# Kernel optimization log

Hardware: AMD Instinct MI355X
Metric: run time of the kernel (lower is better)

The kernel has to match this reference:

```python
import jax, jax.numpy as jnp
import numpy as np

D_MODEL = 1024
M = 4
NUM_EXPERTS = 8
TOP_K = 2
B, T = 2, 2048


def setup_inputs() -> dict:
    key = jax.random.key(0)
    ks = jax.random.split(key, 4)
    d_ff = D_MODEL * M
    x = jax.random.normal(ks[0], (B, T, D_MODEL), dtype=jnp.float32)
    # torch nn.Linear(d_model, num_experts, bias=False): stored here as (D, E) so logits = x @ gate_w
    gate_w = jax.random.normal(ks[1], (D_MODEL, NUM_EXPERTS), dtype=jnp.float32) * 0.02
    w1 = jax.random.normal(ks[2], (NUM_EXPERTS, D_MODEL, d_ff), dtype=jnp.float32) * 0.02
    b1 = jnp.zeros((NUM_EXPERTS, d_ff), dtype=jnp.float32)
    w2 = jax.random.normal(ks[3], (NUM_EXPERTS, d_ff, D_MODEL), dtype=jnp.float32) * 0.02
    b2 = jnp.zeros((NUM_EXPERTS, D_MODEL), dtype=jnp.float32)
    return {"x": x, "gate_w": gate_w, "w1": w1, "b1": b1, "w2": w2, "b2": b2}


def reference(x, gate_w, w1, b1, w2, b2):
    Bb, Tt, D = x.shape
    E = w1.shape[0]
    N = Bb * Tt
    # gating: top-k logits -> softmax over the k selected experts
    logits = jnp.einsum('btd,de->bte', x, gate_w)               # (B,T,E)
    top_v, top_i = jax.lax.top_k(logits, TOP_K)                 # (B,T,K)
    top_w = jax.nn.softmax(top_v, axis=-1)                      # (B,T,K)

    xf = x.reshape(N, D)
    idx = top_i.reshape(N, TOP_K)
    wts = top_w.reshape(N, TOP_K)
    # dense combine weights: comb[n, e] = sum_k wts[n,k] * [idx[n,k]==e]
    comb = jnp.zeros((N, E), dtype=x.dtype).at[jnp.arange(N)[:, None], idx].add(wts)

    # per-expert dense 2-layer MLP (exact erf GELU, matching torch F.gelu default),
    # combined with gate weights (zero weight == token not routed to expert).
    out = jnp.zeros((N, D), dtype=x.dtype)
    for e in range(E):
        h = jax.nn.gelu(xf @ w1[e] + b1[e], approximate=False)  # (N, D*M)
        out = out + comb[:, e:e + 1] * (h @ w2[e] + b2[e])      # (N, D)
    return out.reshape(Bb, Tt, D)
```

## Files before the change

### kernel.cpp

```cpp
#include <hip/hip_runtime.h>
#include <hip/hip_bf16.h>
#include <math.h>

#define D_MODEL 1024
#define D_FF    4096
#define NEXP    8
#define NTOK    4096
#define NROUTED 8192
#define MAXJOBS 40

typedef __attribute__((ext_vector_type(8))) short bf16x8;
typedef __attribute__((ext_vector_type(4))) float f32x4;
typedef __attribute__((ext_vector_type(4))) unsigned short us4;

#define WS_CNT   0
#define WS_CNT2  64
#define WS_OFF   128
#define WS_JOBS  192
#define WS_TI    512
#define WS_TW    (WS_TI + NTOK*2*4)
#define WS_TOK   (WS_TW + NTOK*2*4)
#define WS_GWT   (WS_TOK + NROUTED*4)
#define WS_XG    (((WS_GWT + NROUTED*4) + 255) & ~255)
#define WS_H     (WS_XG + (size_t)NROUTED*D_MODEL*2)
#define WS_WT    (WS_H + (size_t)NROUTED*D_FF*2)
#define WS_WT2   (WS_WT + (size_t)NEXP*D_FF*D_MODEL*2)
#define WS_END   (WS_WT2 + (size_t)NEXP*D_FF*D_MODEL*2)

__device__ __forceinline__ unsigned short f2bf(float f){
  union { float f; unsigned u; } a; a.f = f;
  unsigned u = a.u;
  u = u + 0x7FFF + ((u >> 16) & 1);
  return (unsigned short)(u >> 16);
}

__device__ __forceinline__ void gload_lds16(const void* g, void* l){
  __builtin_amdgcn_global_load_lds((const __attribute__((address_space(1))) void*)g,
                                   (__attribute__((address_space(3))) void*)l, 16, 0, 0);
}

__global__ void moe_gate_kernel(const float* __restrict__ x, const float* __restrict__ gw,
                                int* cnt, int* __restrict__ ti, float* __restrict__ tw){
  int n = blockIdx.x*4 + (threadIdx.x >> 6);
  int lane = threadIdx.x & 63;
  const float* xr = x + (size_t)n * D_MODEL;
  float acc[NEXP];
  #pragma unroll
  for (int e=0;e<NEXP;e++) acc[e] = 0.f;
  for (int d=lane; d<D_MODEL; d+=64){
    float xv = xr[d];
    #pragma unroll
    for (int e=0;e<NEXP;e++) acc[e] += xv * gw[d*NEXP + e];
  }
  #pragma unroll
  for (int e=0;e<NEXP;e++){
    #pragma unroll
    for (int o=32;o;o>>=1) acc[e] += __shfl_down(acc[e], o, 64);
  }
  if (lane == 0){
    int i0 = 0; float v0 = acc[0];
    #pragma unroll
    for (int e=1;e<NEXP;e++) if (acc[e] > v0){ v0 = acc[e]; i0 = e; }
    int i1 = -1; float v1 = -1e30f;
    #pragma unroll
    for (int e=0;e<NEXP;e++) if (e != i0 && acc[e] > v1){ v1 = acc[e]; i1 = e; }
    float p = expf(v1 - v0);
    float inv = 1.f / (1.f + p);
    ti[n*2] = i0; ti[n*2+1] = i1;
    tw[n*2] = inv; tw[n*2+1] = p * inv;
    atomicAdd(&cnt[i0], 1); atomicAdd(&cnt[i1], 1);
  }
}

__global__ void moe_prefix_kernel(const int* __restrict__ cnt, int* __restrict__ off,
                                  int* __restrict__ jobs){
  if (threadIdx.x == 0){
    int s = 0;
    for (int e=0;e<NEXP;e++){ off[e] = s; s += cnt[e]; }
    off[NEXP] = s;
    int idx = 0;
    for (int e=0;e<NEXP;e++){
      int ns = (cnt[e] + 255) >> 8;
      for (int q=0;q<ns;q++) jobs[1+idx++] = (e<<16) | q;
    }
    jobs[0] = idx;
  }
}

__device__ __forceinline__ void assign_body(
    int n, const float* __restrict__ x, const int* __restrict__ ti,
    const float* __restrict__ tw, const int* __restrict__ off,
    int* cnt2, int* __restrict__ tok, float* __restrict__ gwt,
    unsigned short* __restrict__ Xg){
  __shared__ int ss[2];
  if (threadIdx.x == 0){
    int i0 = ti[n*2], i1 = ti[n*2+1];
    int s0 = off[i0] + atomicAdd(&cnt2[i0], 1);
    int s1 = off[i1] + atomicAdd(&cnt2[i1], 1);
    tok[s0] = n; tok[s1] = n;
    gwt[s0] = tw[n*2]; gwt[s1] = tw[n*2+1];
    ss[0] = s0; ss[1] = s1;
  }
  __syncthreads();
  int s0 = ss[0], s1 = ss[1];
  int t = threadIdx.x;
  f32x4 v = *(const f32x4*)(x + (size_t)n * D_MODEL + t*4);
  us4 pk = { f2bf(v.x), f2bf(v.y), f2bf(v.z), f2bf(v.w) };
  __builtin_nontemporal_store(pk, (us4*)(Xg + (size_t)s0 * D_MODEL + t*4));
  __builtin_nontemporal_store(pk, (us4*)(Xg + (size_t)s1 * D_MODEL + t*4));
}

__device__ __forceinline__ void transpose_tile(
    int idx, int gtid, float (*tile)[65],
    const float* __restrict__ W, unsigned short* __restrict__ Wt, int K, int F){
  int fpe = F >> 6, kpe = K >> 6;
  int e = idx / (fpe*kpe), rem = idx % (fpe*kpe);
  int f0 = (rem % fpe) * 64, k0 = (rem / fpe) * 64;
  const float* Wb = W + (size_t)e * K * F;
  unsigned short* Wtb = Wt + (size_t)e * F * K;
  #pragma unroll
  for (int i=0;i<4;i++){
    int q = i*256 + gtid;
    int r = q >> 4, c4 = (q & 15) * 4;
    f32x4 v = __builtin_nontemporal_load((const f32x4*)(Wb + (size_t)(k0 + r) * F + f0 + c4));
    tile[r][c4] = v.x; tile[r][c4+1] = v.y; tile[r][c4+2] = v.z; tile[r][c4+3] = v.w;
  }
  __syncthreads();
  #pragma unroll
  for (int i=0;i<4;i++){
    int q = i*256 + gtid;
    int f = q >> 4, k4 = (q & 15) * 4;
    us4 pk = { f2bf(tile[k4][f]), f2bf(tile[k4+1][f]), f2bf(tile[k4+2][f]), f2bf(tile[k4+3][f]) };
    __builtin_nontemporal_store(pk, (us4*)(Wtb + (size_t)(f0 + f) * K + k0 + k4));
  }
}

__global__ __launch_bounds__(256) void transpose_bf16_kernel(
    const float* W, unsigned short* Wt, int K, int F){
  __shared__ float tile[64][65];
  transpose_tile(blockIdx.x, threadIdx.x, tile, W, Wt, K, F);
}

__global__ __launch_bounds__(256) void moe_fusedA_kernel(
    const float* __restrict__ x, const int* __restrict__ ti, const float* __restrict__ tw,
    const int* __restrict__ off, int* cnt2, int* __restrict__ tok, float* __restrict__ gwt,
    unsigned short* __restrict__ Xg,
    const float* __restrict__ w1, unsigned short* __restrict__ Wt1){
  int b = blockIdx.x;
  if (b < NTOK){
    assign_body(b, x, ti, tw, off, cnt2, tok, gwt, Xg);
  } else {
    __shared__ float tile[64][65];
    transpose_tile(b - NTOK, threadIdx.x, tile, w1, Wt1, D_MODEL, D_FF);
  }
}

template<int MODE>
__global__ __launch_bounds__(1024) void moe_gemm_kernel(
    char* __restrict__ wsb, const unsigned short* __restrict__ Bt,
    const float* __restrict__ bias, float* __restrict__ out,
    const float* __restrict__ w2src, unsigned short* __restrict__ Wt2)
{
  __shared__ __align__(16) char lds[3*32768];

  if (MODE == 1 && (int)blockIdx.y >= MAXJOBS){
    int slot = ((int)blockIdx.y - MAXJOBS) * (int)gridDim.x + (int)blockIdx.x;
    int g = threadIdx.x >> 8, gtid = threadIdx.x & 255;
    float (*tiles)[64][65] = (float(*)[64][65])lds;
    transpose_tile(slot*4 + g, gtid, tiles[g], w2src, Wt2, D_FF, D_MODEL);
    return;
  }

  const int* jobs = (const int*)(wsb + WS_JOBS);
  if ((int)blockIdx.y >= jobs[0]) return;
  const int jb = jobs[1 + blockIdx.y];
  const int e = jb >> 16;
  const int row0 = (jb & 0xffff) << 8;

  const int* off = (const int*)(wsb + WS_OFF);
  const int n0 = off[e];
  const int ne = off[e+1] - n0;

  constexpr int K  = (MODE==1) ? D_MODEL : D_FF;
  constexpr int NT = (MODE==1) ? 32 : 64;
  const int bx     = (MODE==1) ? blockIdx.x : (blockIdx.x & 3);
  const int kchunk = (MODE==1) ? 0 : (blockIdx.x >> 2);
  const int n_off  = bx * 256;
  const size_t kcb = (size_t)kchunk * 4096;

  const unsigned short* Ag = (const unsigned short*)(wsb + (MODE==1 ? (size_t)WS_XG : (size_t)WS_H));

  const int tid = threadIdx.x, lane = tid & 63, w = tid >> 6;
  const int wr = w >> 2, wc = w & 3;

  const int rA   = w*16 + (lane >> 2);
  const int qs   = ((lane & 3) ^ ((rA >> 1) & 3)) << 4;
  int grA = row0 + rA; if (grA >= ne) grA = ne - 1;
  const char* aSrc = (const char*)(Ag + (size_t)(n0 + grA) * K) + kcb + qs;
  const char* bSrc = (const char*)(Bt + (size_t)e * D_FF * D_MODEL + (size_t)(n_off + rA) * K) + kcb + qs;
  const int dA = w*1024, dB = 16384 + w*1024;

  const int q0 = lane >> 4;
  int aoff[4], boff[4];
  #pragma unroll
  for (int mi=0; mi<4; mi++){
    int row = wr*64 + mi*16 + (lane & 15);
    aoff[mi] = row*64 + ((q0 ^ ((row>>1)&3)) << 4);
  }
  #pragma unroll
  for (int ni=0; ni<4; ni++){
    int col = wc*64 + ni*16 + (lane & 15);
    boff[ni] = 16384 + col*64 + ((q0 ^ ((col>>1)&3)) << 4);
  }

  f32x4 acc[4][4];
  #pragma unroll
  for (int i=0;i<4;i++)
    #pragma unroll
    for (int j=0;j<4;j++) acc[i][j] = (f32x4){0.f,0.f,0.f,0.f};

  #define STAGE(tt, ss) { \
    gload_lds16(aSrc + (size_t)(tt)*64, lds + (ss)*32768 + dA); \
    gload_lds16(bSrc + (size_t)(tt)*64, lds + (ss)*32768 + dB); }

  STAGE(0, 0);
  STAGE(1, 1);

  for (int t = 0; t < NT; ++t){
    if (t < NT-1) asm volatile("s_waitcnt vmcnt(2)" ::: "memory");
    else          asm volatile("s_waitcnt vmcnt(0)" ::: "memory");
    __builtin_amdgcn_s_barrier();
    __builtin_amdgcn_sched_barrier(0);

    if (t + 2 < NT) STAGE(t + 2, (t + 2) % 3);

    const char* base = lds + (t % 3) * 32768;
    bf16x8 a[4], b[4];
    #pragma unroll
    for (int mi=0; mi<4; mi++) a[mi] = *(const bf16x8*)(base + aoff[mi]);
    #pragma unroll
    for (int ni=0; ni<4; ni++) b[ni] = *(const bf16x8*)(base + boff[ni]);

    asm volatile("s_waitcnt lgkmcnt(0)" ::: "memory");
    __builtin_amdgcn_sched_barrier(0);
    __builtin_amdgcn_s_setprio(1);
    #pragma unroll
    for (int ni=0; ni<4; ni++)
      #pragma unroll
      for (int mi=0; mi<4; mi++)
        acc[mi][ni] = __builtin_amdgcn_mfma_f32_16x16x32_bf16(a[mi], b[ni], acc[mi][ni], 0, 0, 0);
    __builtin_amdgcn_s_setprio(0);
    __builtin_amdgcn_sched_barrier(0);
  }
  #undef STAGE

  if (MODE == 1){
    const float* b1 = bias + (size_t)e * D_FF;
    unsigned short* H = (unsigned short*)(wsb + (size_t)WS_H);
    #pragma unroll
    for (int mi=0; mi<4; mi++){
      int rbase = wr*64 + mi*16 + ((lane>>4)<<2);
      #pragma unroll
      for (int rr=0;rr<4;rr++){
        int lrow = rbase + rr;
        if (row0 + lrow < ne){
          size_t hb = (size_t)(n0 + row0 + lrow) * D_FF;
          #pragma unroll
          for (int ni=0; ni<4; ni++){
            int gcol = n_off + wc*64 + ni*16 + (lane&15);
            float v = acc[mi][ni][rr] + b1[gcol];
            v = 0.5f * v * (1.f + erff(v * 0.70710678118654752f));
            __builtin_nontemporal_store(f2bf(v), H + hb + gcol);
          }
        }
      }
    }
  } else {
    const float* b2 = bias + (size_t)e * D_MODEL;
    const int* tok = (const int*)(wsb + WS_TOK);
    const float* gwt = (const float*)(wsb + WS_GWT);
    #pragma unroll
    for (int mi=0; mi<4; mi++){
      int rbase = wr*64 + mi*16 + ((lane>>4)<<2);
      #pragma unroll
      for (int rr=0;rr<4;rr++){
        int lrow = rbase + rr;
        if (row0 + lrow < ne){
          int slot = n0 + row0 + lrow;
          int tk = tok[slot];
          float g = gwt[slot];
          float* orow = out + (size_t)tk * D_MODEL;
          #pragma unroll
          for (int ni=0; ni<4; ni++){
            int gcol = n_off + wc*64 + ni*16 + (lane&15);
            float bb = (kchunk == 0) ? b2[gcol] : 0.f;
            atomicAdd(orow + gcol, (acc[mi][ni][rr] + bb) * g);
          }
        }
      }
    }
  }
}

extern "C" void kernel_launch(void* const* d_in, const int* in_sizes, int n_in,
                              void* d_out, int out_size, void* d_ws, size_t ws_size,
                              hipStream_t stream){
  const float* x   = (const float*)d_in[0];
  const float* gw  = (const float*)d_in[1];
  const float* w1  = (const float*)d_in[2];
  const float* b1  = (const float*)d_in[3];
  const float* w2  = (const float*)d_in[4];
  const float* b2  = (const float*)d_in[5];
  float* out = (float*)d_out;
  char* ws = (char*)d_ws;
  unsigned short* Wt1 = (unsigned short*)(ws + (size_t)WS_WT);
  unsigned short* Wt2 = (unsigned short*)(ws + (size_t)WS_WT2);

  hipMemsetAsync(ws, 0, 512, stream);
  hipMemsetAsync(out, 0, (size_t)NTOK * D_MODEL * sizeof(float), stream);

  moe_gate_kernel<<<NTOK/4, 256, 0, stream>>>(x, gw, (int*)(ws+WS_CNT),
                                              (int*)(ws+WS_TI), (float*)(ws+WS_TW));
  moe_prefix_kernel<<<1, 64, 0, stream>>>((const int*)(ws+WS_CNT), (int*)(ws+WS_OFF),
                                          (int*)(ws+WS_JOBS));
  moe_fusedA_kernel<<<NTOK + 8192, 256, 0, stream>>>(
      x, (const int*)(ws+WS_TI), (const float*)(ws+WS_TW), (const int*)(ws+WS_OFF),
      (int*)(ws+WS_CNT2), (int*)(ws+WS_TOK), (float*)(ws+WS_GWT),
      (unsigned short*)(ws + (size_t)WS_XG), w1, Wt1);

  if (ws_size >= (size_t)WS_END){
    moe_gemm_kernel<1><<<dim3(D_FF/256, MAXJOBS + 128), 1024, 0, stream>>>(ws, Wt1, b1, out, w2, Wt2);
    moe_gemm_kernel<2><<<dim3((D_MODEL/256)*2, MAXJOBS), 1024, 0, stream>>>(ws, Wt2, b2, out, nullptr, nullptr);
  } else {
    moe_gemm_kernel<1><<<dim3(D_FF/256, MAXJOBS), 1024, 0, stream>>>(ws, Wt1, b1, out, nullptr, nullptr);
    transpose_bf16_kernel<<<8192, 256, 0, stream>>>(w2, Wt1, D_FF, D_MODEL);
    moe_gemm_kernel<2><<<dim3((D_MODEL/256)*2, MAXJOBS), 1024, 0, stream>>>(ws, Wt1, b2, out, nullptr, nullptr);
  }
}
```

Before: 541.7 us.

## Restructure expert GEMM to 8-wave blocks with 128-wide K double-buffered ping-pong

The expert GEMM kernel moves from 16 waves with a triple-buffered 64-wide K step to 8 waves (two blocks per CU) with a double-buffered 128-wide K step. Each wave now computes a 128x64 sub-tile, and the per-step work is split into four MFMA phases with barriers, so the next A and B tiles are staged while earlier phases compute. The aim is more MFMA work per LDS byte and per barrier, plus overlap of loads with compute, in the style of a ping-pong schedule. The cost is more accumulator registers and many more barriers per step, and the transpose side-blocks are re-gridded to match the smaller blocks.

```diff
diff --git a/kernel.cpp b/kernel.cpp
--- a/kernel.cpp
+++ b/kernel.cpp
@@ -156,18 +156,18 @@
 }
 
 template<int MODE>
-__global__ __launch_bounds__(1024) void moe_gemm_kernel(
+__global__ __launch_bounds__(512, 2) void moe_gemm_kernel(
     char* __restrict__ wsb, const unsigned short* __restrict__ Bt,
     const float* __restrict__ bias, float* __restrict__ out,
     const float* __restrict__ w2src, unsigned short* __restrict__ Wt2)
 {
-  __shared__ __align__(16) char lds[3*32768];
+  __shared__ __align__(16) char lds[2*65536];
 
   if (MODE == 1 && (int)blockIdx.y >= MAXJOBS){
     int slot = ((int)blockIdx.y - MAXJOBS) * (int)gridDim.x + (int)blockIdx.x;
     int g = threadIdx.x >> 8, gtid = threadIdx.x & 255;
     float (*tiles)[64][65] = (float(*)[64][65])lds;
-    transpose_tile(slot*4 + g, gtid, tiles[g], w2src, Wt2, D_FF, D_MODEL);
+    transpose_tile(slot*2 + g, gtid, tiles[g], w2src, Wt2, D_FF, D_MODEL);
     return;
   }
 
@@ -182,7 +182,7 @@
   const int ne = off[e+1] - n0;
 
   constexpr int K  = (MODE==1) ? D_MODEL : D_FF;
-  constexpr int NT = (MODE==1) ? 32 : 64;
+  constexpr int NT = (MODE==1) ? 16 : 32;
   const int bx     = (MODE==1) ? blockIdx.x : (blockIdx.x & 3);
   const int kchunk = (MODE==1) ? 0 : (blockIdx.x >> 2);
   const int n_off  = bx * 256;
@@ -191,75 +191,146 @@
   const unsigned short* Ag = (const unsigned short*)(wsb + (MODE==1 ? (size_t)WS_XG : (size_t)WS_H));
 
   const int tid = threadIdx.x, lane = tid & 63, w = tid >> 6;
-  const int wr = w >> 2, wc = w & 3;
-
-  const int rA   = w*16 + (lane >> 2);
-  const int qs   = ((lane & 3) ^ ((rA >> 1) & 3)) << 4;
-  int grA = row0 + rA; if (grA >= ne) grA = ne - 1;
-  const char* aSrc = (const char*)(Ag + (size_t)(n0 + grA) * K) + kcb + qs;
-  const char* bSrc = (const char*)(Bt + (size_t)e * D_FF * D_MODEL + (size_t)(n_off + rA) * K) + kcb + qs;
-  const int dA = w*1024, dB = 16384 + w*1024;
-
-  const int q0 = lane >> 4;
-  int aoff[4], boff[4];
-  #pragma unroll
-  for (int mi=0; mi<4; mi++){
-    int row = wr*64 + mi*16 + (lane & 15);
-    aoff[mi] = row*64 + ((q0 ^ ((row>>1)&3)) << 4);
-  }
-  #pragma unroll
-  for (int ni=0; ni<4; ni++){
-    int col = wc*64 + ni*16 + (lane & 15);
-    boff[ni] = 16384 + col*64 + ((q0 ^ ((col>>1)&3)) << 4);
-  }
-
-  f32x4 acc[4][4];
-  #pragma unroll
-  for (int i=0;i<4;i++)
+  const int wrM = w >> 2, wcN = w & 3;
+  const int l15 = lane & 15, q16 = (lane >> 4) << 4;
+
+  const int arow   = lane >> 3;
+  const int achunk = ((lane & 7) ^ arow) << 4;
+  const char* aP[4]; const char* bP[4];
+  #pragma unroll
+  for (int i=0;i<4;i++){
+    int r = (w*4 + i)*8 + arow;
+    int gr = row0 + r; if (gr >= ne) gr = ne - 1;
+    aP[i] = (const char*)(Ag + (size_t)(n0 + gr) * K) + kcb + achunk;
+    bP[i] = (const char*)(Bt + (size_t)e * D_FF * D_MODEL + (size_t)(n_off + r) * K) + kcb + achunk;
+  }
+  const int dstA = w*4096;
+
+  #define STAGE_A(tt, bb) { \
+    size_t kb = (size_t)(tt)*128; \
+    char* d = lds + (bb)*65536 + dstA; \
+    _Pragma("unroll") \
+    for (int i=0;i<4;i++) gload_lds16(aP[i] + kb, d + i*1024); }
+  #define STAGE_B(tt, bb) { \
+    size_t kb = (size_t)(tt)*128; \
+    char* d = lds + (bb)*65536 + 32768 + dstA; \
+    _Pragma("unroll") \
+    for (int i=0;i<4;i++) gload_lds16(bP[i] + kb, d + i*1024); }
+
+  f32x4 acc[8][4];
+  #pragma unroll
+  for (int i=0;i<8;i++)
     #pragma unroll
     for (int j=0;j<4;j++) acc[i][j] = (f32x4){0.f,0.f,0.f,0.f};
 
-  #define STAGE(tt, ss) { \
-    gload_lds16(aSrc + (size_t)(tt)*64, lds + (ss)*32768 + dA); \
-    gload_lds16(bSrc + (size_t)(tt)*64, lds + (ss)*32768 + dB); }
-
-  STAGE(0, 0);
-  STAGE(1, 1);
+  STAGE_A(0, 0); STAGE_B(0, 0);
+  asm volatile("s_waitcnt vmcnt(0)" ::: "memory");
+  __builtin_amdgcn_s_barrier();
 
   for (int t = 0; t < NT; ++t){
-    if (t < NT-1) asm volatile("s_waitcnt vmcnt(2)" ::: "memory");
-    else          asm volatile("s_waitcnt vmcnt(0)" ::: "memory");
-    __builtin_amdgcn_s_barrier();
-    __builtin_amdgcn_sched_barrier(0);
-
-    if (t + 2 < NT) STAGE(t + 2, (t + 2) % 3);
-
-    const char* base = lds + (t % 3) * 32768;
-    bf16x8 a[4], b[4];
-    #pragma unroll
-    for (int mi=0; mi<4; mi++) a[mi] = *(const bf16x8*)(base + aoff[mi]);
-    #pragma unroll
-    for (int ni=0; ni<4; ni++) b[ni] = *(const bf16x8*)(base + boff[ni]);
-
+    const char* base = lds + (t & 1) * 65536;
+    const int nb = (t & 1) ^ 1;
+    bf16x8 aF[2][4], bL[2][2], bH[2][2];
+
+    #pragma unroll
+    for (int kk=0; kk<2; ++kk){
+      #pragma unroll
+      for (int mi=0; mi<4; mi++){
+        int row = wrM*128 + mi*16 + l15;
+        aF[kk][mi] = *(const bf16x8*)(base + (row<<7) + (((kk<<6)+q16) ^ ((row&7)<<4)));
+      }
+      #pragma unroll
+      for (int ni=0; ni<2; ni++){
+        int col = wcN*64 + ni*16 + l15;
+        bL[kk][ni] = *(const bf16x8*)(base + 32768 + (col<<7) + (((kk<<6)+q16) ^ ((col&7)<<4)));
+      }
+    }
+    if (t + 1 < NT) STAGE_A(t+1, nb);
+    __builtin_amdgcn_sched_barrier(0);
+    __builtin_amdgcn_s_barrier();
     asm volatile("s_waitcnt lgkmcnt(0)" ::: "memory");
     __builtin_amdgcn_sched_barrier(0);
     __builtin_amdgcn_s_setprio(1);
     #pragma unroll
-    for (int ni=0; ni<4; ni++)
-      #pragma unroll
-      for (int mi=0; mi<4; mi++)
-        acc[mi][ni] = __builtin_amdgcn_mfma_f32_16x16x32_bf16(a[mi], b[ni], acc[mi][ni], 0, 0, 0);
+    for (int kk=0; kk<2; ++kk)
+      #pragma unroll
+      for (int ni=0; ni<2; ni++)
+        #pragma unroll
+        for (int mi=0; mi<4; mi++)
+          acc[mi][ni] = __builtin_amdgcn_mfma_f32_16x16x32_bf16(aF[kk][mi], bL[kk][ni], acc[mi][ni], 0, 0, 0);
     __builtin_amdgcn_s_setprio(0);
     __builtin_amdgcn_sched_barrier(0);
-  }
-  #undef STAGE
+    __builtin_amdgcn_s_barrier();
+
+    #pragma unroll
+    for (int kk=0; kk<2; ++kk)
+      #pragma unroll
+      for (int ni=0; ni<2; ni++){
+        int col = wcN*64 + (ni+2)*16 + l15;
+        bH[kk][ni] = *(const bf16x8*)(base + 32768 + (col<<7) + (((kk<<6)+q16) ^ ((col&7)<<4)));
+      }
+    if (t + 1 < NT) STAGE_B(t+1, nb);
+    __builtin_amdgcn_sched_barrier(0);
+    __builtin_amdgcn_s_barrier();
+    asm volatile("s_waitcnt lgkmcnt(0)" ::: "memory");
+    __builtin_amdgcn_sched_barrier(0);
+    __builtin_amdgcn_s_setprio(1);
+    #pragma unroll
+    for (int kk=0; kk<2; ++kk)
+      #pragma unroll
+      for (int ni=0; ni<2; ni++)
+        #pragma unroll
+        for (int mi=0; mi<4; mi++)
+          acc[mi][ni+2] = __builtin_amdgcn_mfma_f32_16x16x32_bf16(aF[kk][mi], bH[kk][ni], acc[mi][ni+2], 0, 0, 0);
+    __builtin_amdgcn_s_setprio(0);
+    __builtin_amdgcn_sched_barrier(0);
+    __builtin_amdgcn_s_barrier();
+
+    #pragma unroll
+    for (int kk=0; kk<2; ++kk)
+      #pragma unroll
+      for (int mi=0; mi<4; mi++){
+        int row = wrM*128 + (mi+4)*16 + l15;
+        aF[kk][mi] = *(const bf16x8*)(base + (row<<7) + (((kk<<6)+q16) ^ ((row&7)<<4)));
+      }
+    __builtin_amdgcn_sched_barrier(0);
+    __builtin_amdgcn_s_barrier();
+    asm volatile("s_waitcnt lgkmcnt(0)" ::: "memory");
+    __builtin_amdgcn_sched_barrier(0);
+    __builtin_amdgcn_s_setprio(1);
+    #pragma unroll
+    for (int kk=0; kk<2; ++kk)
+      #pragma unroll
+      for (int ni=0; ni<2; ni++)
+        #pragma unroll
+        for (int mi=0; mi<4; mi++)
+          acc[mi+4][ni] = __builtin_amdgcn_mfma_f32_16x16x32_bf16(aF[kk][mi], bL[kk][ni], acc[mi+4][ni], 0, 0, 0);
+    __builtin_amdgcn_s_setprio(0);
+    __builtin_amdgcn_sched_barrier(0);
+    __builtin_amdgcn_s_barrier();
+
+    __builtin_amdgcn_s_setprio(1);
+    #pragma unroll
+    for (int kk=0; kk<2; ++kk)
+      #pragma unroll
+      for (int ni=0; ni<2; ni++)
+        #pragma unroll
+        for (int mi=0; mi<4; mi++)
+          acc[mi+4][ni+2] = __builtin_amdgcn_mfma_f32_16x16x32_bf16(aF[kk][mi], bH[kk][ni], acc[mi+4][ni+2], 0, 0, 0);
+    __builtin_amdgcn_s_setprio(0);
+    __builtin_amdgcn_sched_barrier(0);
+    if (t + 1 < NT) asm volatile("s_waitcnt vmcnt(0)" ::: "memory");
+    __builtin_amdgcn_s_barrier();
+  }
+  #undef STAGE_A
+  #undef STAGE_B
 
   if (MODE == 1){
     const float* b1 = bias + (size_t)e * D_FF;
     unsigned short* H = (unsigned short*)(wsb + (size_t)WS_H);
     #pragma unroll
-    for (int mi=0; mi<4; mi++){
-      int rbase = wr*64 + mi*16 + ((lane>>4)<<2);
+    for (int mi=0; mi<8; mi++){
+      int rbase = wrM*128 + mi*16 + ((lane>>4)<<2);
       #pragma unroll
       for (int rr=0;rr<4;rr++){
         int lrow = rbase + rr;
@@ -267,7 +338,7 @@
           size_t hb = (size_t)(n0 + row0 + lrow) * D_FF;
           #pragma unroll
           for (int ni=0; ni<4; ni++){
-            int gcol = n_off + wc*64 + ni*16 + (lane&15);
+            int gcol = n_off + wcN*64 + ni*16 + l15;
             float v = acc[mi][ni][rr] + b1[gcol];
             v = 0.5f * v * (1.f + erff(v * 0.70710678118654752f));
             __builtin_nontemporal_store(f2bf(v), H + hb + gcol);
@@ -280,8 +351,8 @@
     const int* tok = (const int*)(wsb + WS_TOK);
     const float* gwt = (const float*)(wsb + WS_GWT);
     #pragma unroll
-    for (int mi=0; mi<4; mi++){
-      int rbase = wr*64 + mi*16 + ((lane>>4)<<2);
+    for (int mi=0; mi<8; mi++){
+      int rbase = wrM*128 + mi*16 + ((lane>>4)<<2);
       #pragma unroll
       for (int rr=0;rr<4;rr++){
         int lrow = rbase + rr;
@@ -292,7 +363,7 @@
           float* orow = out + (size_t)tk * D_MODEL;
           #pragma unroll
           for (int ni=0; ni<4; ni++){
-            int gcol = n_off + wc*64 + ni*16 + (lane&15);
+            int gcol = n_off + wcN*64 + ni*16 + l15;
             float bb = (kchunk == 0) ? b2[gcol] : 0.f;
             atomicAdd(orow + gcol, (acc[mi][ni][rr] + bb) * g);
           }
@@ -329,11 +400,11 @@
       (unsigned short*)(ws + (size_t)WS_XG), w1, Wt1);
 
   if (ws_size >= (size_t)WS_END){
-    moe_gemm_kernel<1><<<dim3(D_FF/256, MAXJOBS + 128), 1024, 0, stream>>>(ws, Wt1, b1, out, w2, Wt2);
-    moe_gemm_kernel<2><<<dim3((D_MODEL/256)*2, MAXJOBS), 1024, 0, stream>>>(ws, Wt2, b2, out, nullptr, nullptr);
+    moe_gemm_kernel<1><<<dim3(D_FF/256, MAXJOBS + 256), 512, 0, stream>>>(ws, Wt1, b1, out, w2, Wt2);
+    moe_gemm_kernel<2><<<dim3((D_MODEL/256)*2, MAXJOBS), 512, 0, stream>>>(ws, Wt2, b2, out, nullptr, nullptr);
   } else {
-    moe_gemm_kernel<1><<<dim3(D_FF/256, MAXJOBS), 1024, 0, stream>>>(ws, Wt1, b1, out, nullptr, nullptr);
+    moe_gemm_kernel<1><<<dim3(D_FF/256, MAXJOBS), 512, 0, stream>>>(ws, Wt1, b1, out, nullptr, nullptr);
     transpose_bf16_kernel<<<8192, 256, 0, stream>>>(w2, Wt1, D_FF, D_MODEL);
-    moe_gemm_kernel<2><<<dim3((D_MODEL/256)*2, MAXJOBS), 1024, 0, stream>>>(ws, Wt1, b2, out, nullptr, nullptr);
-  }
-}
+    moe_gemm_kernel<2><<<dim3((D_MODEL/256)*2, MAXJOBS), 512, 0, stream>>>(ws, Wt1, b2, out, nullptr, nullptr);
+  }
+}
```

After: 598.7 us. +10.5%, slower.
